# Performance work log

Measured on AMD Instinct MI355X. Metric: run time of the kernel, lower is better.

The kernel has to match this reference:

```python
import jax, jax.numpy as jnp
import numpy as np

TOPK = 2

def setup_inputs() -> dict:
    key = jax.random.key(0)
    ks = jax.random.split(key, 5)
    B, S, D, H, E = 2, 4096, 1024, 2048, 8
    x = jax.random.normal(ks[0], (B, S, D), dtype=jnp.float32)
    router_w = jax.random.normal(ks[1], (E, D), dtype=jnp.float32) * 0.02
    w1 = jax.random.normal(ks[2], (E, D, H), dtype=jnp.float32) * 0.02
    w3 = jax.random.normal(ks[3], (E, D, H), dtype=jnp.float32) * 0.02
    w2 = jax.random.normal(ks[4], (E, H, D), dtype=jnp.float32) * 0.02
    return {"x": x, "router_w": router_w, "w1": w1, "w3": w3, "w2": w2}

def reference(x, router_w, w1, w3, w2):
    B, S, D = x.shape
    E = router_w.shape[0]
    xf = x.reshape(-1, D)                      # [T, D]
    T = xf.shape[0]
    logits = (xf @ router_w.T).astype(jnp.float32)      # [T, E]
    weights, indices = jax.lax.top_k(logits, TOPK)      # [T, k]
    weights = jax.nn.softmax(weights, axis=-1).astype(x.dtype)
    prob = jax.nn.softmax(logits, axis=-1)              # [T, E] fp32
    P = prob.mean(axis=0).astype(x.dtype)               # [E]
    mask = jnp.zeros((T, E), jnp.float32).at[jnp.arange(T)[:, None], indices].set(1.0)
    f = mask.mean(axis=0).astype(x.dtype)               # [E]
    aux_loss = E * jnp.sum(f * P)
    out = jnp.zeros_like(xf)
    for e in range(E):
        # combine weight for expert e per token (0 if not routed here)
        coef = jnp.sum(jnp.where(indices == e, weights, jnp.zeros_like(weights)), axis=-1)  # [T]
        h = jax.nn.silu(xf @ w1[e]) * (xf @ w3[e])      # [T, H] SwiGLU
        out = out + coef[:, None] * (h @ w2[e])         # masked combine == gather/scatter
    return out.reshape(B, S, D), aux_loss
```

## Files before the change

kernel.cpp:

```cpp
#include <hip/hip_runtime.h>
#include <hip/hip_bf16.h>

#define TT 8192
#define DD 1024
#define HH 2048
#define EE 8

typedef __bf16 bf16x8 __attribute__((ext_vector_type(8)));
typedef float floatx4 __attribute__((ext_vector_type(4)));
typedef short shortx8 __attribute__((ext_vector_type(8)));

__device__ __forceinline__ short f2bf(float f) {
  unsigned u = __float_as_uint(f);
  u += 0x7fffu + ((u >> 16) & 1u);
  return (short)(u >> 16);
}

__device__ __forceinline__ void gld16(const void* g, void* l) {
  __builtin_amdgcn_global_load_lds((const __attribute__((address_space(1))) void*)g,
                                   (__attribute__((address_space(3))) void*)l, 16, 0, 0);
}

__global__ __launch_bounds__(256) void router_kernel(
    const float* __restrict__ x, const float* __restrict__ rw,
    int* __restrict__ cpad, float* __restrict__ ppad,
    int* __restrict__ list_token, float* __restrict__ list_coef,
    short* __restrict__ xb)
{
  __shared__ int   sE0[32], sE1[32], lcnt[EE], sbase[EE], lp0[32], lp1[32];
  __shared__ float sG0[32], sG1[32], sP[EE];
  const int tid = threadIdx.x;
  if (tid < EE) { sP[tid] = 0.f; lcnt[tid] = 0; }
  __syncthreads();
  const int lane = tid & 63, wv = tid >> 6;
  const int t0 = blockIdx.x * 32;
  for (int ti = 0; ti < 8; ++ti) {
    const int s = wv * 8 + ti;
    const int t = t0 + s;
    float sc[EE];
#pragma unroll
    for (int e = 0; e < EE; ++e) sc[e] = 0.f;
#pragma unroll
    for (int j = 0; j < 4; ++j) {
      float4 xv = *(const float4*)(x + (size_t)t * DD + j * 256 + lane * 4);
#pragma unroll
      for (int e = 0; e < EE; ++e) {
        float4 rv = *(const float4*)(rw + e * DD + j * 256 + lane * 4);
        sc[e] += xv.x * rv.x + xv.y * rv.y + xv.z * rv.z + xv.w * rv.w;
      }
      if (xb) {
        short4 sv = make_short4(f2bf(xv.x), f2bf(xv.y), f2bf(xv.z), f2bf(xv.w));
        *(short4*)(xb + (size_t)t * DD + j * 256 + lane * 4) = sv;
      }
    }
#pragma unroll
    for (int off = 32; off > 0; off >>= 1)
#pragma unroll
      for (int e = 0; e < EE; ++e)
        sc[e] += __shfl_down(sc[e], off);
    if (lane == 0) {
      int i0 = 0; float l0 = sc[0];
      for (int e = 1; e < EE; ++e) if (sc[e] > l0) { l0 = sc[e]; i0 = e; }
      int i1 = -1; float l1 = -3.4e38f;
      for (int e = 0; e < EE; ++e) if (e != i0 && sc[e] > l1) { l1 = sc[e]; i1 = e; }
      const float g0 = 1.f / (1.f + __expf(l1 - l0));
      float pr[EE]; float sum = 0.f;
      for (int e = 0; e < EE; ++e) { pr[e] = __expf(sc[e] - l0); sum += pr[e]; }
      const float inv = 1.f / sum;
      for (int e = 0; e < EE; ++e) atomicAdd(&sP[e], pr[e] * inv);
      sE0[s] = i0; sE1[s] = i1; sG0[s] = g0; sG1[s] = 1.f - g0;
    }
  }
  __syncthreads();
  if (tid < 32) {
    lp0[tid] = atomicAdd(&lcnt[sE0[tid]], 1);
    lp1[tid] = atomicAdd(&lcnt[sE1[tid]], 1);
  }
  __syncthreads();
  if (tid < EE) {
    sbase[tid] = atomicAdd(&cpad[tid * 16], lcnt[tid]);
    atomicAdd(&ppad[tid * 16], sP[tid]);
  }
  __syncthreads();
  if (tid < 32) {
    int e0 = sE0[tid], e1 = sE1[tid], t = t0 + tid;
    int p0 = sbase[e0] + lp0[tid];
    int p1 = sbase[e1] + lp1[tid];
    list_token[e0 * TT + p0] = t; list_coef[e0 * TT + p0] = sG0[tid];
    list_token[e1 * TT + p1] = t; list_coef[e1 * TT + p1] = sG1[tid];
  }
}

__global__ void aux_kernel(const int* __restrict__ cpad, const float* __restrict__ ppad,
                           int* __restrict__ offsets, float* __restrict__ out_aux)
{
  if (threadIdx.x == 0) {
    float aux = 0.f; int off = 0;
    for (int e = 0; e < EE; ++e) {
      aux += ((float)cpad[e * 16] / (float)TT) * (ppad[e * 16] / (float)TT);
      offsets[e] = off; off += cpad[e * 16];
    }
    *out_aux = aux * (float)EE;
  }
}

__global__ __launch_bounds__(256) void convt_kernel(const float* __restrict__ in, short* __restrict__ out,
                                                    int R, int C)
{
  __shared__ short T[64 * 74];
  const int t = threadIdx.x;
  const size_t eoff = (size_t)blockIdx.z * R * C;
  in += eoff; out += eoff;
  const int c0 = blockIdx.x * 64, r0 = blockIdx.y * 64;
#pragma unroll
  for (int p = 0; p < 4; ++p) {
    int r = p * 16 + (t >> 4), c4 = (t & 15) * 4;
    float4 v = *(const float4*)(in + (size_t)(r0 + r) * C + c0 + c4);
    short4 s = make_short4(f2bf(v.x), f2bf(v.y), f2bf(v.z), f2bf(v.w));
    *(short4*)&T[r * 74 + c4] = s;
  }
  __syncthreads();
#pragma unroll
  for (int q = 0; q < 2; ++q) {
    int u = q * 256 + t;
    int oc = u >> 3, k8 = (u & 7) * 8;
    shortx8 s;
#pragma unroll
    for (int j = 0; j < 8; ++j) s[j] = T[(k8 + j) * 74 + oc];
    *(shortx8*)&out[(size_t)(c0 + oc) * R + r0 + k8] = s;
  }
}

__global__ __launch_bounds__(256, 2) void g1f_kernel(
    const short* __restrict__ xb, const short* __restrict__ w1t, const short* __restrict__ w3t,
    const int* __restrict__ cpad, const int* __restrict__ offsets,
    const int* __restrict__ list_token, short* __restrict__ Hbuf)
{
  const int e = blockIdx.z, rb = blockIdx.y, nb = blockIdx.x;
  const int cnt = cpad[e * 16];
  if (rb * 128 >= cnt) return;
  __shared__ short Asm[128 * 32];
  __shared__ short B1sm[128 * 32];
  __shared__ short B3sm[128 * 32];
  const int tid = threadIdx.x, lane = tid & 63, wv = tid >> 6;
  const int wm = (wv >> 1) * 64, wn = (wv & 1) * 64;
  const int quad = lane >> 4, l16 = lane & 15;
  floatx4 acc1[4][4] = {{{0.f}}};
  floatx4 acc3[4][4] = {{{0.f}}};
  const int rlo = wv * 32 + (lane >> 2);
  int toklo, tokhi;
  {
    int glo = rb * 128 + rlo, ghi = glo + 16;
    toklo = (glo < cnt) ? list_token[e * TT + glo] : list_token[e * TT];
    tokhi = (ghi < cnt) ? list_token[e * TT + ghi] : list_token[e * TT];
  }
  const char* aglo = (const char*)(xb + (size_t)toklo * DD) + (lane & 3) * 16;
  const char* aghi = (const char*)(xb + (size_t)tokhi * DD) + (lane & 3) * 16;
  char* al = (char*)Asm + wv * 2048;
  const int brow = wv * 32 + (lane >> 2);
  const int bcb = (lane & 3) * 16;
  const char* w1g = (const char*)(w1t + (size_t)e * HH * DD + (size_t)(nb * 128 + brow) * DD) + bcb;
  const char* w3g = (const char*)(w3t + (size_t)e * HH * DD + (size_t)(nb * 128 + brow) * DD) + bcb;
  char* b1l = (char*)B1sm + wv * 2048;
  char* b3l = (char*)B3sm + wv * 2048;
  int aro[4], bro[4];
#pragma unroll
  for (int mi = 0; mi < 4; ++mi) aro[mi] = (wm + mi * 16 + l16) * 32 + quad * 8;
#pragma unroll
  for (int ni = 0; ni < 4; ++ni) bro[ni] = (wn + ni * 16 + l16) * 32 + quad * 8;

  for (int k0 = 0; k0 < DD; k0 += 32) {
    __syncthreads();
    gld16(aglo + (size_t)k0 * 2, al);
    gld16(aghi + (size_t)k0 * 2, al + 1024);
    gld16(w1g + (size_t)k0 * 2, b1l);
    gld16(w1g + (size_t)k0 * 2 + 16 * DD * 2, b1l + 1024);
    gld16(w3g + (size_t)k0 * 2, b3l);
    gld16(w3g + (size_t)k0 * 2 + 16 * DD * 2, b3l + 1024);
    __syncthreads();
    bf16x8 af[4], b1f[4], b3f[4];
#pragma unroll
    for (int mi = 0; mi < 4; ++mi) af[mi] = *(const bf16x8*)&Asm[aro[mi]];
#pragma unroll
    for (int ni = 0; ni < 4; ++ni) {
      b1f[ni] = *(const bf16x8*)&B1sm[bro[ni]];
      b3f[ni] = *(const bf16x8*)&B3sm[bro[ni]];
    }
#pragma unroll
    for (int mi = 0; mi < 4; ++mi)
#pragma unroll
      for (int ni = 0; ni < 4; ++ni) {
        acc1[mi][ni] = __builtin_amdgcn_mfma_f32_16x16x32_bf16(af[mi], b1f[ni], acc1[mi][ni], 0, 0, 0);
        acc3[mi][ni] = __builtin_amdgcn_mfma_f32_16x16x32_bf16(af[mi], b3f[ni], acc3[mi][ni], 0, 0, 0);
      }
  }
  const int off = offsets[e];
#pragma unroll
  for (int mi = 0; mi < 4; ++mi)
#pragma unroll
    for (int r = 0; r < 4; ++r) {
      int row = wm + mi * 16 + quad * 4 + r;
      int grow = rb * 128 + row;
      if (grow < cnt) {
        size_t rowbase = (size_t)(off + grow) * HH + (size_t)nb * 128 + wn;
#pragma unroll
        for (int ni = 0; ni < 4; ++ni) {
          float a = acc1[mi][ni][r], b = acc3[mi][ni][r];
          float h = a / (1.f + __expf(-a)) * b;
          Hbuf[rowbase + ni * 16 + l16] = f2bf(h);
        }
      }
    }
}

__global__ __launch_bounds__(256, 2) void g2f_kernel(
    const short* __restrict__ Hbuf, const short* __restrict__ w2t,
    const int* __restrict__ cpad, const int* __restrict__ offsets,
    const int* __restrict__ list_token, const float* __restrict__ list_coef,
    float* __restrict__ out)
{
  const int e = blockIdx.z, rb = blockIdx.y, nb = blockIdx.x;
  const int cnt = cpad[e * 16];
  if (rb * 128 >= cnt) return;
  __shared__ short Asm[128 * 32];
  __shared__ short Bsm[128 * 32];
  const int tid = threadIdx.x, lane = tid & 63, wv = tid >> 6;
  const int wm = (wv >> 1) * 64, wn = (wv & 1) * 64;
  const int quad = lane >> 4, l16 = lane & 15;
  floatx4 acc[4][4] = {{{0.f}}};
  const int off = offsets[e];
  const int qrow = wv * 32 + (lane >> 2);
  const int qcb = (lane & 3) * 16;
  const char* ag = (const char*)(Hbuf + (size_t)(off + rb * 128 + qrow) * HH) + qcb;
  const char* bg = (const char*)(w2t + (size_t)e * DD * HH + (size_t)(nb * 128 + qrow) * HH) + qcb;
  char* al = (char*)Asm + wv * 2048;
  char* bl = (char*)Bsm + wv * 2048;
  int aro[4], bro[4];
#pragma unroll
  for (int mi = 0; mi < 4; ++mi) aro[mi] = (wm + mi * 16 + l16) * 32 + quad * 8;
#pragma unroll
  for (int ni = 0; ni < 4; ++ni) bro[ni] = (wn + ni * 16 + l16) * 32 + quad * 8;

  for (int k0 = 0; k0 < HH; k0 += 32) {
    __syncthreads();
    gld16(ag + (size_t)k0 * 2, al);
    gld16(ag + (size_t)k0 * 2 + 16 * HH * 2, al + 1024);
    gld16(bg + (size_t)k0 * 2, bl);
    gld16(bg + (size_t)k0 * 2 + 16 * HH * 2, bl + 1024);
    __syncthreads();
    bf16x8 af[4], bf[4];
#pragma unroll
    for (int mi = 0; mi < 4; ++mi) af[mi] = *(const bf16x8*)&Asm[aro[mi]];
#pragma unroll
    for (int ni = 0; ni < 4; ++ni) bf[ni] = *(const bf16x8*)&Bsm[bro[ni]];
#pragma unroll
    for (int mi = 0; mi < 4; ++mi)
#pragma unroll
      for (int ni = 0; ni < 4; ++ni)
        acc[mi][ni] = __builtin_amdgcn_mfma_f32_16x16x32_bf16(af[mi], bf[ni], acc[mi][ni], 0, 0, 0);
  }
#pragma unroll
  for (int mi = 0; mi < 4; ++mi)
#pragma unroll
    for (int r = 0; r < 4; ++r) {
      int row = wm + mi * 16 + quad * 4 + r;
      int grow = rb * 128 + row;
      if (grow < cnt) {
        int tokid = list_token[e * TT + grow];
        float coef = list_coef[e * TT + grow];
        float* orow = out + (size_t)tokid * DD + (size_t)nb * 128 + wn;
#pragma unroll
        for (int ni = 0; ni < 4; ++ni)
          atomicAdd(&orow[ni * 16 + l16], coef * acc[mi][ni][r]);
      }
    }
}

__global__ __launch_bounds__(256, 2) void g1s_kernel(
    const float* __restrict__ x, const float* __restrict__ w1, const float* __restrict__ w3,
    const int* __restrict__ cpad, const int* __restrict__ offsets,
    const int* __restrict__ list_token, short* __restrict__ Hbuf)
{
  const int e = blockIdx.z, rb = blockIdx.y, nb = blockIdx.x;
  const int cnt = cpad[e * 16];
  if (rb * 128 >= cnt) return;
  __shared__ short Asm[128 * 40];
  __shared__ short B1sm[128 * 40];
  __shared__ short B3sm[128 * 40];
  const int tid = threadIdx.x, lane = tid & 63, wv = tid >> 6;
  const int wm = (wv >> 1) * 64, wn = (wv & 1) * 64;
  const int quad = lane >> 4, l16 = lane & 15;
  floatx4 acc1[4][4] = {{{0.f}}};
  floatx4 acc3[4][4] = {{{0.f}}};
  const int ar = tid >> 3, ak = (tid & 7) * 4;
  const int bp = tid & 63, bq = tid >> 6;
  const int bswz = (bq ^ ((bp >> 2) & 3)) * 8;
  const int bo0 = (2 * bp) * 40 + bswz, bo1 = bo0 + 40;
  int aro[4], bro[4];
#pragma unroll
  for (int mi = 0; mi < 4; ++mi) aro[mi] = (wm + mi * 16 + l16) * 40 + quad * 8;
#pragma unroll
  for (int ni = 0; ni < 4; ++ni) {
    int nl = wn + ni * 16 + l16;
    bro[ni] = nl * 40 + ((quad ^ ((nl >> 3) & 3)) * 8);
  }
  int tok[4];
#pragma unroll
  for (int i = 0; i < 4; ++i) {
    int gr = rb * 128 + ar + 32 * i;
    tok[i] = (gr < cnt) ? list_token[e * TT + gr] : list_token[e * TT];
  }
  const float* w1e = w1 + (size_t)e * DD * HH + (size_t)nb * 128;
  const float* w3e = w3 + (size_t)e * DD * HH + (size_t)nb * 128;
  for (int k0 = 0; k0 < DD; k0 += 32) {
    __syncthreads();
#pragma unroll
    for (int i = 0; i < 4; ++i) {
      int r = ar + 32 * i;
      float4 v = *(const float4*)(x + (size_t)tok[i] * DD + k0 + ak);
      short4 sv = make_short4(f2bf(v.x), f2bf(v.y), f2bf(v.z), f2bf(v.w));
      *(short4*)&Asm[r * 40 + ak] = sv;
    }
    {
      float2 u[8];
#pragma unroll
      for (int j = 0; j < 8; ++j) u[j] = *(const float2*)(w1e + (size_t)(k0 + bq * 8 + j) * HH + 2 * bp);
      shortx8 p0, p1;
#pragma unroll
      for (int j = 0; j < 8; ++j) { p0[j] = f2bf(u[j].x); p1[j] = f2bf(u[j].y); }
      *(shortx8*)&B1sm[bo0] = p0; *(shortx8*)&B1sm[bo1] = p1;
    }
    {
      float2 u[8];
#pragma unroll
      for (int j = 0; j < 8; ++j) u[j] = *(const float2*)(w3e + (size_t)(k0 + bq * 8 + j) * HH + 2 * bp);
      shortx8 p0, p1;
#pragma unroll
      for (int j = 0; j < 8; ++j) { p0[j] = f2bf(u[j].x); p1[j] = f2bf(u[j].y); }
      *(shortx8*)&B3sm[bo0] = p0; *(shortx8*)&B3sm[bo1] = p1;
    }
    __syncthreads();
    bf16x8 af[4], b1f[4], b3f[4];
#pragma unroll
    for (int mi = 0; mi < 4; ++mi) af[mi] = *(const bf16x8*)&Asm[aro[mi]];
#pragma unroll
    for (int ni = 0; ni < 4; ++ni) {
      b1f[ni] = *(const bf16x8*)&B1sm[bro[ni]];
      b3f[ni] = *(const bf16x8*)&B3sm[bro[ni]];
    }
#pragma unroll
    for (int mi = 0; mi < 4; ++mi)
#pragma unroll
      for (int ni = 0; ni < 4; ++ni) {
        acc1[mi][ni] = __builtin_amdgcn_mfma_f32_16x16x32_bf16(af[mi], b1f[ni], acc1[mi][ni], 0, 0, 0);
        acc3[mi][ni] = __builtin_amdgcn_mfma_f32_16x16x32_bf16(af[mi], b3f[ni], acc3[mi][ni], 0, 0, 0);
      }
  }
  const int off = offsets[e];
#pragma unroll
  for (int mi = 0; mi < 4; ++mi)
#pragma unroll
    for (int r = 0; r < 4; ++r) {
      int row = wm + mi * 16 + quad * 4 + r;
      int grow = rb * 128 + row;
      if (grow < cnt) {
        size_t rowbase = (size_t)(off + grow) * HH + (size_t)nb * 128 + wn;
#pragma unroll
        for (int ni = 0; ni < 4; ++ni) {
          float a = acc1[mi][ni][r], b = acc3[mi][ni][r];
          float h = a / (1.f + __expf(-a)) * b;
          Hbuf[rowbase + ni * 16 + l16] = f2bf(h);
        }
      }
    }
}

__global__ __launch_bounds__(256, 2) void g2s_kernel(
    const short* __restrict__ Hbuf, const float* __restrict__ w2,
    const int* __restrict__ cpad, const int* __restrict__ offsets,
    const int* __restrict__ list_token, const float* __restrict__ list_coef,
    float* __restrict__ out)
{
  const int e = blockIdx.z, rb = blockIdx.y, nb = blockIdx.x;
  const int cnt = cpad[e * 16];
  if (rb * 128 >= cnt) return;
  __shared__ short Asm[128 * 40];
  __shared__ short Bsm[128 * 40];
  const int tid = threadIdx.x, lane = tid & 63, wv = tid >> 6;
  const int wm = (wv >> 1) * 64, wn = (wv & 1) * 64;
  const int quad = lane >> 4, l16 = lane & 15;
  floatx4 acc[4][4] = {{{0.f}}};
  const int ar = tid >> 3, ak = (tid & 7) * 4;
  const int bp = tid & 63, bq = tid >> 6;
  const int bswz = (bq ^ ((bp >> 2) & 3)) * 8;
  const int bo0 = (2 * bp) * 40 + bswz, bo1 = bo0 + 40;
  int aro[4], bro[4];
#pragma unroll
  for (int mi = 0; mi < 4; ++mi) aro[mi] = (wm + mi * 16 + l16) * 40 + quad * 8;
#pragma unroll
  for (int ni = 0; ni < 4; ++ni) {
    int nl = wn + ni * 16 + l16;
    bro[ni] = nl * 40 + ((quad ^ ((nl >> 3) & 3)) * 8);
  }
  const int off = offsets[e];
  size_t hrow[4];
#pragma unroll
  for (int i = 0; i < 4; ++i) {
    int gr = rb * 128 + ar + 32 * i;
    int cg = (gr < cnt) ? gr : (cnt - 1);
    hrow[i] = (size_t)(off + cg) * HH;
  }
  const float* w2e = w2 + (size_t)e * HH * DD + (size_t)nb * 128;
  for (int k0 = 0; k0 < HH; k0 += 32) {
    __syncthreads();
#pragma unroll
    for (int i = 0; i < 4; ++i) {
      int r = ar + 32 * i;
      short4 sv = *(const short4*)(Hbuf + hrow[i] + k0 + ak);
      *(short4*)&Asm[r * 40 + ak] = sv;
    }
    {
      float2 u[8];
#pragma unroll
      for (int j = 0; j < 8; ++j) u[j] = *(const float2*)(w2e + (size_t)(k0 + bq * 8 + j) * DD + 2 * bp);
      shortx8 p0, p1;
#pragma unroll
      for (int j = 0; j < 8; ++j) { p0[j] = f2bf(u[j].x); p1[j] = f2bf(u[j].y); }
      *(shortx8*)&Bsm[bo0] = p0; *(shortx8*)&Bsm[bo1] = p1;
    }
    __syncthreads();
    bf16x8 af[4], bf[4];
#pragma unroll
    for (int mi = 0; mi < 4; ++mi) af[mi] = *(const bf16x8*)&Asm[aro[mi]];
#pragma unroll
    for (int ni = 0; ni < 4; ++ni) bf[ni] = *(const bf16x8*)&Bsm[bro[ni]];
#pragma unroll
    for (int mi = 0; mi < 4; ++mi)
#pragma unroll
      for (int ni = 0; ni < 4; ++ni)
        acc[mi][ni] = __builtin_amdgcn_mfma_f32_16x16x32_bf16(af[mi], bf[ni], acc[mi][ni], 0, 0, 0);
  }
#pragma unroll
  for (int mi = 0; mi < 4; ++mi)
#pragma unroll
    for (int r = 0; r < 4; ++r) {
      int row = wm + mi * 16 + quad * 4 + r;
      int grow = rb * 128 + row;
      if (grow < cnt) {
        int tokid = list_token[e * TT + grow];
        float coef = list_coef[e * TT + grow];
        float* orow = out + (size_t)tokid * DD + (size_t)nb * 128 + wn;
#pragma unroll
        for (int ni = 0; ni < 4; ++ni)
          atomicAdd(&orow[ni * 16 + l16], coef * acc[mi][ni][r]);
      }
    }
}

extern "C" void kernel_launch(void* const* d_in, const int* in_sizes, int n_in,
                              void* d_out, int out_size, void* d_ws, size_t ws_size,
                              hipStream_t stream)
{
  const float* x  = (const float*)d_in[0];
  const float* rw = (const float*)d_in[1];
  const float* w1 = (const float*)d_in[2];
  const float* w3 = (const float*)d_in[3];
  const float* w2 = (const float*)d_in[4];
  float* out = (float*)d_out;

  char* ws = (char*)d_ws;
  int*   cpad      = (int*)(ws + 0);
  float* ppad      = (float*)(ws + 512);
  int*   offsets   = (int*)(ws + 1024);
  int*   list_tok  = (int*)(ws + 4096);
  float* list_coef = (float*)(ws + 4096 + EE * TT * 4);

  const size_t OFF_W1T = 1u << 20;
  const size_t OFF_W3T = OFF_W1T + ((size_t)EE * DD * HH * 2);
  const size_t OFF_XBF = OFF_W3T + ((size_t)EE * DD * HH * 2);
  const size_t OFF_HB  = OFF_XBF + ((size_t)TT * DD * 2);
  const size_t NEED    = OFF_HB + ((size_t)(2 * TT + 128) * HH * 2);

  hipMemsetAsync(ws, 0, 1024, stream);
  hipMemsetAsync(d_out, 0, (size_t)TT * DD * sizeof(float), stream);

  const bool fast = (ws_size >= NEED);
  short* XBF = fast ? (short*)(ws + OFF_XBF) : nullptr;

  router_kernel<<<256, 256, 0, stream>>>(x, rw, cpad, ppad, list_tok, list_coef, XBF);
  aux_kernel<<<1, 64, 0, stream>>>(cpad, ppad, offsets, out + (size_t)TT * DD);

  if (fast) {
    short* W1T = (short*)(ws + OFF_W1T);
    short* W3T = (short*)(ws + OFF_W3T);
    short* HB  = (short*)(ws + OFF_HB);
    convt_kernel<<<dim3(HH / 64, DD / 64, EE), 256, 0, stream>>>(w1, W1T, DD, HH);
    convt_kernel<<<dim3(HH / 64, DD / 64, EE), 256, 0, stream>>>(w3, W3T, DD, HH);
    g1f_kernel<<<dim3(HH / 128, TT / 128, EE), 256, 0, stream>>>(XBF, W1T, W3T, cpad, offsets, list_tok, HB);
    convt_kernel<<<dim3(DD / 64, HH / 64, EE), 256, 0, stream>>>(w2, W1T, HH, DD);
    g2f_kernel<<<dim3(DD / 128, TT / 128, EE), 256, 0, stream>>>(HB, W1T, cpad, offsets, list_tok, list_coef, out);
  } else {
    short* HB = (short*)(ws + (1 << 20));
    g1s_kernel<<<dim3(HH / 128, TT / 128, EE), 256, 0, stream>>>(x, w1, w3, cpad, offsets, list_tok, HB);
    g2s_kernel<<<dim3(DD / 128, TT / 128, EE), 256, 0, stream>>>(HB, w2, cpad, offsets, list_tok, list_coef, out);
  }
}
```

Baseline: 595.8 us.

## Rewrite expert GEMMs with 256x256 tiles, double-buffered LDS pipeline and interleaved W1/W3

Replaces both expert GEMM kernels with 512-thread, 256x256-tile kernels built on a shared mma_core. The core double-buffers a 128 KB LDS region with XOR-swizzled layout, interleaves async global->LDS loads with MFMA phases under explicit barriers, waitcnts and setprio. W1 and W3 are transposed into one interleaved matrix (32-column groups alternated) so a single GEMM produces gate and up columns together for the SwiGLU epilogue. The aim is more data reuse per tile and less load stall, at the cost of one block per wave-heavy 128 KB LDS footprint, more padding waste for the per-expert token counts, and fragile hand scheduling.

```diff
diff --git a/kernel.cpp b/kernel.cpp
--- a/kernel.cpp
+++ b/kernel.cpp
@@ -105,12 +105,12 @@
 }
 
 __global__ __launch_bounds__(256) void convt_kernel(const float* __restrict__ in, short* __restrict__ out,
-                                                    int R, int C)
+                                                    int R, int C, int mode)
 {
   __shared__ short T[64 * 74];
   const int t = threadIdx.x;
-  const size_t eoff = (size_t)blockIdx.z * R * C;
-  in += eoff; out += eoff;
+  in  += (size_t)blockIdx.z * R * C;
+  out += (size_t)blockIdx.z * R * C * (mode ? 2 : 1);
   const int c0 = blockIdx.x * 64, r0 = blockIdx.y * 64;
 #pragma unroll
   for (int p = 0; p < 4; ++p) {
@@ -127,93 +127,140 @@
     shortx8 s;
 #pragma unroll
     for (int j = 0; j < 8; ++j) s[j] = T[(k8 + j) * 74 + oc];
-    *(shortx8*)&out[(size_t)(c0 + oc) * R + r0 + k8] = s;
-  }
-}
-
-__global__ __launch_bounds__(256, 2) void g1f_kernel(
-    const short* __restrict__ xb, const short* __restrict__ w1t, const short* __restrict__ w3t,
+    int c = c0 + oc;
+    int grow = (mode == 0) ? c : (2 * (c & ~31) + (c & 31) + ((mode == 2) ? 32 : 0));
+    *(shortx8*)&out[(size_t)grow * R + r0 + k8] = s;
+  }
+}
+
+
+#define PH_BAR()  { __builtin_amdgcn_s_barrier(); __builtin_amdgcn_sched_barrier(0); }
+#define WAITL0()  { asm volatile("s_waitcnt lgkmcnt(0)" ::: "memory"); __builtin_amdgcn_sched_barrier(0); }
+#define WAITVN(n) { asm volatile("s_waitcnt vmcnt(" #n ")" ::: "memory"); __builtin_amdgcn_sched_barrier(0); }
+
+template<int NT>
+__device__ __forceinline__ void mma_core(char* SM, int tid,
+    const char* a00, const char* a01, const char* a10, const char* a11,
+    const char* b00, const char* b01, const char* b10, const char* b11,
+    floatx4 (&acc)[8][4])
+{
+  const int lane = tid & 63, w = tid >> 6;
+  const int l16 = lane & 15, quad = lane >> 4;
+  const int wm = (w >> 2) & 1, wn = w & 3;
+  const int cx = (((l16 >> 1) & 1) << 4) | (((l16 >> 2) & 1) << 5) | ((l16 & 1) << 6);
+  const int ck0 = (quad * 16) ^ cx;
+  const int arb = (wm * 128 + l16) * 128;
+  const int brb = 32768 + (wn * 64 + l16) * 128;
+  const int wq = w * 2048;
+
+#define SA_(u,h,p0,p1) { gld16((p0) + (size_t)(u) * 128, SM + (((u) & 1) << 16) + (h) * 16384 + wq); \
+                         gld16((p1) + (size_t)(u) * 128, SM + (((u) & 1) << 16) + (h) * 16384 + wq + 1024); }
+#define SB_(u,h,p0,p1) { gld16((p0) + (size_t)(u) * 128, SM + (((u) & 1) << 16) + 32768 + (h) * 16384 + wq); \
+                         gld16((p1) + (size_t)(u) * 128, SM + (((u) & 1) << 16) + 32768 + (h) * 16384 + wq + 1024); }
+#define LA_(mi) { a[mi][0] = *(const bf16x8*)(SM + cur + arb + (mi) * 2048 + ck0); \
+                  a[mi][1] = *(const bf16x8*)(SM + cur + arb + (mi) * 2048 + (ck0 ^ 64)); }
+#define LB_(ni) { b[ni][0] = *(const bf16x8*)(SM + cur + brb + (ni) * 2048 + ck0); \
+                  b[ni][1] = *(const bf16x8*)(SM + cur + brb + (ni) * 2048 + (ck0 ^ 64)); }
+#define MM_(mi,ni) { acc[mi][ni] = __builtin_amdgcn_mfma_f32_16x16x32_bf16(a[mi][0], b[ni][0], acc[mi][ni], 0, 0, 0); \
+                     acc[mi][ni] = __builtin_amdgcn_mfma_f32_16x16x32_bf16(a[mi][1], b[ni][1], acc[mi][ni], 0, 0, 0); }
+
+  SA_(0, 0, a00, a01); SA_(0, 1, a10, a11);
+  SB_(0, 0, b00, b01); SB_(0, 1, b10, b11);
+  SA_(1, 0, a00, a01); SA_(1, 1, a10, a11);
+  WAITVN(4);
+  __builtin_amdgcn_s_barrier();
+  __builtin_amdgcn_sched_barrier(0);
+
+#pragma unroll 2
+  for (int t = 0; t < NT; ++t) {
+    const int cur = (t & 1) << 16;
+    bf16x8 a[8][2], b[4][2];
+    LA_(0) LA_(1) LA_(2) LA_(3) LB_(0) LB_(1)
+    if (t + 1 < NT) SB_(t + 1, 0, b00, b01);
+    PH_BAR(); WAITL0();
+    __builtin_amdgcn_s_setprio(1);
+    MM_(0,0) MM_(1,0) MM_(2,0) MM_(3,0) MM_(0,1) MM_(1,1) MM_(2,1) MM_(3,1)
+    __builtin_amdgcn_s_setprio(0);
+    PH_BAR();
+    LA_(4) LA_(5) LA_(6) LA_(7) LB_(2) LB_(3)
+    if (t + 1 < NT) SB_(t + 1, 1, b10, b11);
+    PH_BAR(); WAITL0();
+    __builtin_amdgcn_s_setprio(1);
+    MM_(4,2) MM_(5,2) MM_(6,2) MM_(7,2) MM_(4,3) MM_(5,3) MM_(6,3) MM_(7,3)
+    __builtin_amdgcn_s_setprio(0);
+    PH_BAR();
+    if (t + 2 < NT) SA_(t + 2, 0, a00, a01);
+    PH_BAR();
+    __builtin_amdgcn_s_setprio(1);
+    MM_(0,2) MM_(1,2) MM_(2,2) MM_(3,2) MM_(0,3) MM_(1,3) MM_(2,3) MM_(3,3)
+    __builtin_amdgcn_s_setprio(0);
+    PH_BAR();
+    if (t + 2 < NT) SA_(t + 2, 1, a10, a11);
+    PH_BAR();
+    __builtin_amdgcn_s_setprio(1);
+    MM_(4,0) MM_(5,0) MM_(6,0) MM_(7,0) MM_(4,1) MM_(5,1) MM_(6,1) MM_(7,1)
+    __builtin_amdgcn_s_setprio(0);
+    if (t + 2 < NT) { WAITVN(4); } else { WAITVN(0); }
+    PH_BAR();
+  }
+#undef SA_
+#undef SB_
+#undef LA_
+#undef LB_
+#undef MM_
+}
+
+__global__ __launch_bounds__(512, 2) void g1p_kernel(
+    const short* __restrict__ xb, const short* __restrict__ w13t,
     const int* __restrict__ cpad, const int* __restrict__ offsets,
     const int* __restrict__ list_token, short* __restrict__ Hbuf)
 {
   const int e = blockIdx.z, rb = blockIdx.y, nb = blockIdx.x;
   const int cnt = cpad[e * 16];
-  if (rb * 128 >= cnt) return;
-  __shared__ short Asm[128 * 32];
-  __shared__ short B1sm[128 * 32];
-  __shared__ short B3sm[128 * 32];
-  const int tid = threadIdx.x, lane = tid & 63, wv = tid >> 6;
-  const int wm = (wv >> 1) * 64, wn = (wv & 1) * 64;
-  const int quad = lane >> 4, l16 = lane & 15;
-  floatx4 acc1[4][4] = {{{0.f}}};
-  floatx4 acc3[4][4] = {{{0.f}}};
-  const int rlo = wv * 32 + (lane >> 2);
-  int toklo, tokhi;
-  {
-    int glo = rb * 128 + rlo, ghi = glo + 16;
-    toklo = (glo < cnt) ? list_token[e * TT + glo] : list_token[e * TT];
-    tokhi = (ghi < cnt) ? list_token[e * TT + ghi] : list_token[e * TT];
-  }
-  const char* aglo = (const char*)(xb + (size_t)toklo * DD) + (lane & 3) * 16;
-  const char* aghi = (const char*)(xb + (size_t)tokhi * DD) + (lane & 3) * 16;
-  char* al = (char*)Asm + wv * 2048;
-  const int brow = wv * 32 + (lane >> 2);
-  const int bcb = (lane & 3) * 16;
-  const char* w1g = (const char*)(w1t + (size_t)e * HH * DD + (size_t)(nb * 128 + brow) * DD) + bcb;
-  const char* w3g = (const char*)(w3t + (size_t)e * HH * DD + (size_t)(nb * 128 + brow) * DD) + bcb;
-  char* b1l = (char*)B1sm + wv * 2048;
-  char* b3l = (char*)B3sm + wv * 2048;
-  int aro[4], bro[4];
-#pragma unroll
-  for (int mi = 0; mi < 4; ++mi) aro[mi] = (wm + mi * 16 + l16) * 32 + quad * 8;
-#pragma unroll
-  for (int ni = 0; ni < 4; ++ni) bro[ni] = (wn + ni * 16 + l16) * 32 + quad * 8;
-
-  for (int k0 = 0; k0 < DD; k0 += 32) {
-    __syncthreads();
-    gld16(aglo + (size_t)k0 * 2, al);
-    gld16(aghi + (size_t)k0 * 2, al + 1024);
-    gld16(w1g + (size_t)k0 * 2, b1l);
-    gld16(w1g + (size_t)k0 * 2 + 16 * DD * 2, b1l + 1024);
-    gld16(w3g + (size_t)k0 * 2, b3l);
-    gld16(w3g + (size_t)k0 * 2 + 16 * DD * 2, b3l + 1024);
-    __syncthreads();
-    bf16x8 af[4], b1f[4], b3f[4];
-#pragma unroll
-    for (int mi = 0; mi < 4; ++mi) af[mi] = *(const bf16x8*)&Asm[aro[mi]];
-#pragma unroll
-    for (int ni = 0; ni < 4; ++ni) {
-      b1f[ni] = *(const bf16x8*)&B1sm[bro[ni]];
-      b3f[ni] = *(const bf16x8*)&B3sm[bro[ni]];
-    }
-#pragma unroll
-    for (int mi = 0; mi < 4; ++mi)
-#pragma unroll
-      for (int ni = 0; ni < 4; ++ni) {
-        acc1[mi][ni] = __builtin_amdgcn_mfma_f32_16x16x32_bf16(af[mi], b1f[ni], acc1[mi][ni], 0, 0, 0);
-        acc3[mi][ni] = __builtin_amdgcn_mfma_f32_16x16x32_bf16(af[mi], b3f[ni], acc3[mi][ni], 0, 0, 0);
-      }
-  }
+  if (rb * 256 >= cnt) return;
+  __shared__ char SM[131072];
+  const int tid = threadIdx.x;
+  const int lane = tid & 63, w = tid >> 6;
+  const int srow = lane >> 3;
+  const int scol = (((lane ^ (lane >> 4)) & 1) << 4)
+                 | ((((lane >> 1) ^ (lane >> 5)) & 1) << 5)
+                 | ((((lane >> 2) ^ (lane >> 3)) & 1) << 6);
+  const int* lt = list_token + e * TT;
+  const char* ap[2][2];
+#pragma unroll
+  for (int h = 0; h < 2; ++h)
+#pragma unroll
+    for (int i = 0; i < 2; ++i) {
+      int gr = rb * 256 + h * 128 + (w * 2 + i) * 8 + srow;
+      int tok = (gr < cnt) ? lt[gr] : lt[0];
+      ap[h][i] = (const char*)xb + (size_t)tok * 2048 + scol;
+    }
+  const char* bb = (const char*)w13t + ((size_t)e * 4096 + nb * 256) * 2048
+                 + (size_t)(w * 16 + srow) * 2048 + scol;
+  floatx4 acc[8][4] = {};
+  mma_core<16>(SM, tid, ap[0][0], ap[0][1], ap[1][0], ap[1][1],
+               bb, bb + 8 * 2048, bb + 128 * 2048, bb + 136 * 2048, acc);
   const int off = offsets[e];
-#pragma unroll
-  for (int mi = 0; mi < 4; ++mi)
+  const int l16 = lane & 15, quad = lane >> 4;
+  const int wm = (w >> 2) & 1, wn = w & 3;
+#pragma unroll
+  for (int mi = 0; mi < 8; ++mi)
 #pragma unroll
     for (int r = 0; r < 4; ++r) {
-      int row = wm + mi * 16 + quad * 4 + r;
-      int grow = rb * 128 + row;
+      int grow = rb * 256 + wm * 128 + mi * 16 + quad * 4 + r;
       if (grow < cnt) {
-        size_t rowbase = (size_t)(off + grow) * HH + (size_t)nb * 128 + wn;
-#pragma unroll
-        for (int ni = 0; ni < 4; ++ni) {
-          float a = acc1[mi][ni][r], b = acc3[mi][ni][r];
-          float h = a / (1.f + __expf(-a)) * b;
-          Hbuf[rowbase + ni * 16 + l16] = f2bf(h);
+        size_t rowbase = (size_t)(off + grow) * HH + nb * 128 + wn * 32;
+#pragma unroll
+        for (int ni = 0; ni < 2; ++ni) {
+          float aa = acc[mi][ni][r], bbv = acc[mi][ni + 2][r];
+          float hv = aa / (1.f + __expf(-aa)) * bbv;
+          Hbuf[rowbase + ni * 16 + l16] = f2bf(hv);
         }
       }
     }
 }
 
-__global__ __launch_bounds__(256, 2) void g2f_kernel(
+__global__ __launch_bounds__(512, 2) void g2p_kernel(
     const short* __restrict__ Hbuf, const short* __restrict__ w2t,
     const int* __restrict__ cpad, const int* __restrict__ offsets,
     const int* __restrict__ list_token, const float* __restrict__ list_coef,
@@ -221,54 +268,40 @@
 {
   const int e = blockIdx.z, rb = blockIdx.y, nb = blockIdx.x;
   const int cnt = cpad[e * 16];
-  if (rb * 128 >= cnt) return;
-  __shared__ short Asm[128 * 32];
-  __shared__ short Bsm[128 * 32];
-  const int tid = threadIdx.x, lane = tid & 63, wv = tid >> 6;
-  const int wm = (wv >> 1) * 64, wn = (wv & 1) * 64;
-  const int quad = lane >> 4, l16 = lane & 15;
-  floatx4 acc[4][4] = {{{0.f}}};
+  if (rb * 256 >= cnt) return;
+  __shared__ char SM[131072];
+  const int tid = threadIdx.x;
+  const int lane = tid & 63, w = tid >> 6;
+  const int srow = lane >> 3;
+  const int scol = (((lane ^ (lane >> 4)) & 1) << 4)
+                 | ((((lane >> 1) ^ (lane >> 5)) & 1) << 5)
+                 | ((((lane >> 2) ^ (lane >> 3)) & 1) << 6);
   const int off = offsets[e];
-  const int qrow = wv * 32 + (lane >> 2);
-  const int qcb = (lane & 3) * 16;
-  const char* ag = (const char*)(Hbuf + (size_t)(off + rb * 128 + qrow) * HH) + qcb;
-  const char* bg = (const char*)(w2t + (size_t)e * DD * HH + (size_t)(nb * 128 + qrow) * HH) + qcb;
-  char* al = (char*)Asm + wv * 2048;
-  char* bl = (char*)Bsm + wv * 2048;
-  int aro[4], bro[4];
-#pragma unroll
-  for (int mi = 0; mi < 4; ++mi) aro[mi] = (wm + mi * 16 + l16) * 32 + quad * 8;
-#pragma unroll
-  for (int ni = 0; ni < 4; ++ni) bro[ni] = (wn + ni * 16 + l16) * 32 + quad * 8;
-
-  for (int k0 = 0; k0 < HH; k0 += 32) {
-    __syncthreads();
-    gld16(ag + (size_t)k0 * 2, al);
-    gld16(ag + (size_t)k0 * 2 + 16 * HH * 2, al + 1024);
-    gld16(bg + (size_t)k0 * 2, bl);
-    gld16(bg + (size_t)k0 * 2 + 16 * HH * 2, bl + 1024);
-    __syncthreads();
-    bf16x8 af[4], bf[4];
-#pragma unroll
-    for (int mi = 0; mi < 4; ++mi) af[mi] = *(const bf16x8*)&Asm[aro[mi]];
-#pragma unroll
-    for (int ni = 0; ni < 4; ++ni) bf[ni] = *(const bf16x8*)&Bsm[bro[ni]];
-#pragma unroll
-    for (int mi = 0; mi < 4; ++mi)
-#pragma unroll
-      for (int ni = 0; ni < 4; ++ni)
-        acc[mi][ni] = __builtin_amdgcn_mfma_f32_16x16x32_bf16(af[mi], bf[ni], acc[mi][ni], 0, 0, 0);
-  }
-#pragma unroll
-  for (int mi = 0; mi < 4; ++mi)
+  const char* ap[2][2];
+#pragma unroll
+  for (int h = 0; h < 2; ++h)
+#pragma unroll
+    for (int i = 0; i < 2; ++i) {
+      int gr = rb * 256 + h * 128 + (w * 2 + i) * 8 + srow;
+      int cg = (gr < cnt) ? gr : (cnt - 1);
+      ap[h][i] = (const char*)Hbuf + (size_t)(off + cg) * 4096 + scol;
+    }
+  const char* bb = (const char*)w2t + ((size_t)e * DD + nb * 256) * 4096
+                 + (size_t)(w * 16 + srow) * 4096 + scol;
+  floatx4 acc[8][4] = {};
+  mma_core<32>(SM, tid, ap[0][0], ap[0][1], ap[1][0], ap[1][1],
+               bb, bb + 8 * 4096, bb + 128 * 4096, bb + 136 * 4096, acc);
+  const int l16 = lane & 15, quad = lane >> 4;
+  const int wm = (w >> 2) & 1, wn = w & 3;
+#pragma unroll
+  for (int mi = 0; mi < 8; ++mi)
 #pragma unroll
     for (int r = 0; r < 4; ++r) {
-      int row = wm + mi * 16 + quad * 4 + r;
-      int grow = rb * 128 + row;
+      int grow = rb * 256 + wm * 128 + mi * 16 + quad * 4 + r;
       if (grow < cnt) {
         int tokid = list_token[e * TT + grow];
         float coef = list_coef[e * TT + grow];
-        float* orow = out + (size_t)tokid * DD + (size_t)nb * 128 + wn;
+        float* orow = out + (size_t)tokid * DD + nb * 256 + wn * 64;
 #pragma unroll
         for (int ni = 0; ni < 4; ++ni)
           atomicAdd(&orow[ni * 16 + l16], coef * acc[mi][ni][r]);
@@ -491,14 +524,13 @@
   aux_kernel<<<1, 64, 0, stream>>>(cpad, ppad, offsets, out + (size_t)TT * DD);
 
   if (fast) {
-    short* W1T = (short*)(ws + OFF_W1T);
-    short* W3T = (short*)(ws + OFF_W3T);
-    short* HB  = (short*)(ws + OFF_HB);
-    convt_kernel<<<dim3(HH / 64, DD / 64, EE), 256, 0, stream>>>(w1, W1T, DD, HH);
-    convt_kernel<<<dim3(HH / 64, DD / 64, EE), 256, 0, stream>>>(w3, W3T, DD, HH);
-    g1f_kernel<<<dim3(HH / 128, TT / 128, EE), 256, 0, stream>>>(XBF, W1T, W3T, cpad, offsets, list_tok, HB);
-    convt_kernel<<<dim3(DD / 64, HH / 64, EE), 256, 0, stream>>>(w2, W1T, HH, DD);
-    g2f_kernel<<<dim3(DD / 128, TT / 128, EE), 256, 0, stream>>>(HB, W1T, cpad, offsets, list_tok, list_coef, out);
+    short* W13T = (short*)(ws + OFF_W1T);
+    short* HB   = (short*)(ws + OFF_HB);
+    convt_kernel<<<dim3(HH / 64, DD / 64, EE), 256, 0, stream>>>(w1, W13T, DD, HH, 1);
+    convt_kernel<<<dim3(HH / 64, DD / 64, EE), 256, 0, stream>>>(w3, W13T, DD, HH, 2);
+    g1p_kernel<<<dim3(2 * HH / 256, TT / 256, EE), 512, 0, stream>>>(XBF, W13T, cpad, offsets, list_tok, HB);
+    convt_kernel<<<dim3(DD / 64, HH / 64, EE), 256, 0, stream>>>(w2, W13T, HH, DD, 0);
+    g2p_kernel<<<dim3(DD / 256, TT / 256, EE), 512, 0, stream>>>(HB, W13T, cpad, offsets, list_tok, list_coef, out);
   } else {
     short* HB = (short*)(ws + (1 << 20));
     g1s_kernel<<<dim3(HH / 128, TT / 128, EE), 256, 0, stream>>>(x, w1, w3, cpad, offsets, list_tok, HB);
```

New measurement: 626.1 us. +5.1%, slower.
